# Performance work log

Hardware: AMD Instinct MI355X
Metric: run time of the kernel (lower is better)

## Reference

```python
import jax, jax.numpy as jnp
import numpy as np

DIM = 1024
NUM_HEADS = 16
HEAD_DIM = DIM // NUM_HEADS

def setup_inputs() -> dict:
    key = jax.random.key(0)
    ks = jax.random.split(key, 5)
    s = 1.0 / np.sqrt(DIM)
    x = jax.random.normal(ks[0], (2, 2048, DIM), dtype=jnp.float32)
    W_qkv = jax.random.uniform(ks[1], (DIM, 3 * DIM), dtype=jnp.float32, minval=-s, maxval=s)
    b_qkv = jax.random.uniform(ks[2], (3 * DIM,), dtype=jnp.float32, minval=-s, maxval=s)
    W_out = jax.random.uniform(ks[3], (DIM, DIM), dtype=jnp.float32, minval=-s, maxval=s)
    b_out = jax.random.uniform(ks[4], (DIM,), dtype=jnp.float32, minval=-s, maxval=s)
    return {"x": x, "W_qkv": W_qkv, "b_qkv": b_qkv, "W_out": W_out, "b_out": b_out}

def reference(x, W_qkv, b_qkv, W_out, b_out):
    B, S, _ = x.shape
    qkv = x @ W_qkv + b_qkv                       # [B,S,3*dim]
    q, k, v = jnp.split(qkv, 3, axis=-1)
    # [B,S,dim] -> [B,H,S,hd]
    def to_heads(t):
        return t.reshape(B, S, NUM_HEADS, HEAD_DIM).transpose(0, 2, 1, 3)
    q, k, v = to_heads(q), to_heads(k), to_heads(v)
    scale = HEAD_DIM ** -0.5
    scores = jnp.einsum('bhqd,bhkd->bhqk', q, k) * scale
    attn = jax.nn.softmax(scores, axis=-1)
    out = jnp.einsum('bhqk,bhkd->bhqd', attn, v)  # [B,H,S,hd]
    out = out.transpose(0, 2, 1, 3).reshape(B, S, DIM)
    return out @ W_out + b_out
```

## Files before the change

### kernel.cpp

```cpp
#include <hip/hip_runtime.h>
#include <math.h>

#define DIMM    1024
#define NHEADS  16
#define HDIM    64
#define BATCH   2
#define SEQ     2048
#define ROWS    (BATCH*SEQ)

typedef _Float16 f16x8 __attribute__((ext_vector_type(8)));
typedef _Float16 f16x4 __attribute__((ext_vector_type(4)));
typedef float    f32x4 __attribute__((ext_vector_type(4)));
typedef float    f32x16 __attribute__((ext_vector_type(16)));

__device__ inline void gl_lds16(const void* g, void* l) {
    __builtin_amdgcn_global_load_lds(
        (const __attribute__((address_space(1))) void*)g,
        (__attribute__((address_space(3))) void*)l, 16, 0, 0);
}

static __device__ inline f16x8 mkfrag(unsigned a, unsigned b, unsigned c, unsigned d) {
    union { unsigned u[4]; f16x8 v; } x;
    x.u[0] = a; x.u[1] = b; x.u[2] = c; x.u[3] = d;
    return x.v;
}

__device__ void tcvt64(const float* __restrict__ in, _Float16* __restrict__ out,
                       int K, int N, int k0, int n0, float (*tile)[65], int t)
{
    {
        const int c4 = (t & 15) * 4;
        const int r  = t >> 4;
        #pragma unroll
        for (int i = 0; i < 4; i++) {
            const int rr = r + 16 * i;
            float4 v = *(const float4*)(in + (size_t)(k0 + rr) * N + n0 + c4);
            tile[rr][c4] = v.x; tile[rr][c4 + 1] = v.y;
            tile[rr][c4 + 2] = v.z; tile[rr][c4 + 3] = v.w;
        }
    }
    __syncthreads();
    #pragma unroll
    for (int i = 0; i < 2; i++) {
        const int seg = t + 256 * i;
        const int n   = seg >> 3;
        const int kc  = (seg & 7) * 8;
        f16x8 o;
        #pragma unroll
        for (int j = 0; j < 8; j++) o[j] = (_Float16)tile[kc + j][n];
        *(f16x8*)(out + (size_t)(n0 + n) * K + k0 + kc) = o;
    }
}

__global__ __launch_bounds__(256)
void prep_kernel(const float* __restrict__ x, const float* __restrict__ Wqkv,
                 const float* __restrict__ Wout, _Float16* __restrict__ xh,
                 _Float16* __restrict__ wqkvt, _Float16* __restrict__ woutt)
{
    __shared__ float tile[64][65];
    const int bx = blockIdx.x;
    const int t  = threadIdx.x;
    if (bx < 2048) {
        const int i = bx * 256 + t;
        const float4 a = *(const float4*)(x + (size_t)i * 8);
        const float4 b = *(const float4*)(x + (size_t)i * 8 + 4);
        f16x8 o;
        o[0] = (_Float16)a.x; o[1] = (_Float16)a.y; o[2] = (_Float16)a.z; o[3] = (_Float16)a.w;
        o[4] = (_Float16)b.x; o[5] = (_Float16)b.y; o[6] = (_Float16)b.z; o[7] = (_Float16)b.w;
        *(f16x8*)(xh + (size_t)i * 8) = o;
    } else if (bx < 2816) {
        const int id = bx - 2048;
        const int gx = id % 48, gy = id / 48;
        tcvt64(Wqkv, wqkvt, DIMM, 3 * DIMM, gy * 64, gx * 64, tile, t);
    } else {
        const int id = bx - 2816;
        const int gx = id & 15, gy = id >> 4;
        tcvt64(Wout, woutt, DIMM, DIMM, gy * 64, gx * 64, tile, t);
    }
}

__global__ __launch_bounds__(512)
void hgemm256_kernel(const _Float16* __restrict__ A, const _Float16* __restrict__ Bt,
                     const float* __restrict__ bias, _Float16* __restrict__ C,
                     _Float16* __restrict__ vtg, int N, int K)
{
    __shared__ __align__(16) _Float16 lds[65536];

    const int t    = threadIdx.x;
    const int w    = t >> 6, lane = t & 63;
    const int l31  = lane & 31;
    const int hf   = lane >> 5;
    const int l7   = lane & 7;
    const int wm   = w >> 2;
    const int wn   = w & 3;
    const int row0 = blockIdx.y * 256, col0 = blockIdx.x * 256;

    f32x16 acc[4][2];
    #pragma unroll
    for (int mi = 0; mi < 4; mi++)
        #pragma unroll
        for (int ni = 0; ni < 2; ni++)
            #pragma unroll
            for (int r = 0; r < 16; r++) acc[mi][ni][r] = 0.f;

    const _Float16* gA[4];
    const _Float16* gB[4];
    int sofs[4];
    #pragma unroll
    for (int j = 0; j < 4; j++) {
        const int s   = t + 512 * j;
        const int row = s >> 3;
        const int kb  = (s & 7) ^ (row & 7);
        gA[j] = A  + (size_t)(row0 + row) * K + kb * 8;
        gB[j] = Bt + (size_t)(col0 + row) * K + kb * 8;
        sofs[j] = s * 8;
    }

    #pragma unroll
    for (int j = 0; j < 4; j++) gl_lds16(gA[j], lds + sofs[j]);
    #pragma unroll
    for (int j = 0; j < 4; j++) gl_lds16(gB[j], lds + 32768 + sofs[j]);
    #pragma unroll
    for (int j = 0; j < 4; j++) { gA[j] += 64; gB[j] += 64; }

    const int niter = K >> 6;
    #pragma unroll 1
    for (int it = 0; it < niter; it++) {
        const int cur = it & 1;
        __syncthreads();

        if (it + 1 < niter) {
            const int nxt = cur ^ 1;
            #pragma unroll
            for (int j = 0; j < 4; j++) gl_lds16(gA[j], lds + nxt * 16384 + sofs[j]);
            #pragma unroll
            for (int j = 0; j < 4; j++) gl_lds16(gB[j], lds + 32768 + nxt * 16384 + sofs[j]);
            #pragma unroll
            for (int j = 0; j < 4; j++) { gA[j] += 64; gB[j] += 64; }
        }

        const _Float16* AsC = lds + cur * 16384;
        const _Float16* BsC = lds + 32768 + cur * 16384;
        #pragma unroll
        for (int ks = 0; ks < 4; ks++) {
            const int pseg = ((ks * 2 + hf) ^ l7) * 8;
            f16x8 bf0 = *(const f16x8*)(BsC + (wn * 64 +      l31) * 64 + pseg);
            f16x8 bf1 = *(const f16x8*)(BsC + (wn * 64 + 32 + l31) * 64 + pseg);
            #pragma unroll
            for (int mi = 0; mi < 4; mi++) {
                f16x8 af = *(const f16x8*)(AsC + (wm * 128 + mi * 32 + l31) * 64 + pseg);
                acc[mi][0] = __builtin_amdgcn_mfma_f32_32x32x16_f16(af, bf0, acc[mi][0], 0, 0, 0);
                acc[mi][1] = __builtin_amdgcn_mfma_f32_32x32x16_f16(af, bf1, acc[mi][1], 0, 0, 0);
            }
        }
    }

    float bv[2];
    #pragma unroll
    for (int ni = 0; ni < 2; ni++) bv[ni] = bias[col0 + wn * 64 + ni * 32 + l31];

    if (blockIdx.x < 8) {
        #pragma unroll
        for (int mi = 0; mi < 4; mi++)
            #pragma unroll
            for (int ni = 0; ni < 2; ni++) {
                const int col = col0 + wn * 64 + ni * 32 + l31;
                #pragma unroll
                for (int r = 0; r < 16; r++) {
                    const int row = row0 + wm * 128 + mi * 32 + (r & 3) + 8 * (r >> 2) + 4 * hf;
                    C[(size_t)row * N + col] = (_Float16)(acc[mi][ni][r] + bv[ni]);
                }
            }
        return;
    }

    __syncthreads();
    #pragma unroll
    for (int mi = 0; mi < 4; mi++)
        #pragma unroll
        for (int ni = 0; ni < 2; ni++) {
            const int coll = wn * 64 + ni * 32 + l31;
            #pragma unroll
            for (int rq = 0; rq < 4; rq++) {
                f16x4 o;
                #pragma unroll
                for (int ri = 0; ri < 4; ri++) o[ri] = (_Float16)(acc[mi][ni][rq * 4 + ri] + bv[ni]);
                const int sidx = rq + 4 * mi + 16 * wm;
                *(f16x4*)(lds + coll * 256 + ((sidx ^ (coll & 31)) << 3) + 4 * hf) = o;
            }
        }
    __syncthreads();
    {
        const int cl   = t >> 1;
        const int half = t & 1;
        const int head = ((blockIdx.x - 8) << 2) + (cl >> 6);
        const int dv   = cl & 63;
        const int bb   = blockIdx.y >> 3;
        const int key0 = (blockIdx.y & 7) * 256 + half * 128;
        _Float16* dst = vtg + ((size_t)(bb * 16 + head) * 64 + dv) * SEQ + key0;
        #pragma unroll
        for (int c = 0; c < 16; c++) {
            const int cs = half * 16 + c;
            *(f16x8*)(dst + c * 8) = *(const f16x8*)(lds + cl * 256 + ((cs ^ (cl & 31)) << 3));
        }
    }
}

__global__ __launch_bounds__(256)
void hgemm_out_kernel(const _Float16* __restrict__ A, const _Float16* __restrict__ Bt,
                      const float* __restrict__ bias, float* __restrict__ Cout,
                      int N, int K)
{
    constexpr int BM = 64, MI = 2;
    __shared__ _Float16 As[2][BM * 64];
    __shared__ _Float16 Bs[2][128 * 64];

    const int t    = threadIdx.x;
    const int w    = t >> 6, lane = t & 63;
    const int quad = lane >> 4, l16 = lane & 15;
    const int wr   = w >> 1, wc = w & 1;
    const int row0 = blockIdx.y * BM, col0 = blockIdx.x * 128;
    const int sw   = l16 & 7;

    f32x4 acc[MI][4];
    #pragma unroll
    for (int i = 0; i < MI; i++)
        #pragma unroll
        for (int j = 0; j < 4; j++)
            #pragma unroll
            for (int r = 0; r < 4; r++) acc[i][j][r] = 0.f;

    const _Float16* gA[MI];
    int aofs[MI];
    #pragma unroll
    for (int j = 0; j < MI; j++) {
        const int s   = t + 256 * j;
        const int row = s >> 3;
        const int kb  = (s & 7) ^ (row & 7);
        gA[j] = A + (size_t)(row0 + row) * K + kb * 8;
        aofs[j] = s * 8;
    }
    const _Float16* gB[4];
    int bofs[4];
    #pragma unroll
    for (int j = 0; j < 4; j++) {
        const int s   = t + 256 * j;
        const int row = s >> 3;
        const int kb  = (s & 7) ^ (row & 7);
        gB[j] = Bt + (size_t)(col0 + row) * K + kb * 8;
        bofs[j] = s * 8;
    }

    #pragma unroll
    for (int j = 0; j < MI; j++) gl_lds16(gA[j], &As[0][aofs[j]]);
    #pragma unroll
    for (int j = 0; j < 4; j++)  gl_lds16(gB[j], &Bs[0][bofs[j]]);
    #pragma unroll
    for (int j = 0; j < MI; j++) gA[j] += 64;
    #pragma unroll
    for (int j = 0; j < 4; j++)  gB[j] += 64;

    const int niter = K >> 6;
    #pragma unroll 1
    for (int it = 0; it < niter; it++) {
        const int cur = it & 1;
        __syncthreads();

        if (it + 1 < niter) {
            const int nxt = cur ^ 1;
            #pragma unroll
            for (int j = 0; j < MI; j++) gl_lds16(gA[j], &As[nxt][aofs[j]]);
            #pragma unroll
            for (int j = 0; j < 4; j++)  gl_lds16(gB[j], &Bs[nxt][bofs[j]]);
            #pragma unroll
            for (int j = 0; j < MI; j++) gA[j] += 64;
            #pragma unroll
            for (int j = 0; j < 4; j++)  gB[j] += 64;
        }

        const _Float16* AsC = &As[cur][0];
        const _Float16* BsC = &Bs[cur][0];
        f16x8 af[MI][2], bf[4][2];
        #pragma unroll
        for (int i = 0; i < MI; i++) {
            const int arow = wr * (BM / 2) + i * 16 + l16;
            #pragma unroll
            for (int hh = 0; hh < 2; hh++)
                af[i][hh] = *(const f16x8*)(AsC + (arow * 8 + ((hh * 4 + quad) ^ sw)) * 8);
        }
        #pragma unroll
        for (int j = 0; j < 4; j++) {
            const int brow = wc * 64 + j * 16 + l16;
            #pragma unroll
            for (int hh = 0; hh < 2; hh++)
                bf[j][hh] = *(const f16x8*)(BsC + (brow * 8 + ((hh * 4 + quad) ^ sw)) * 8);
        }
        #pragma unroll
        for (int i = 0; i < MI; i++)
            #pragma unroll
            for (int j = 0; j < 4; j++) {
                acc[i][j] = __builtin_amdgcn_mfma_f32_16x16x32_f16(af[i][0], bf[j][0], acc[i][j], 0, 0, 0);
                acc[i][j] = __builtin_amdgcn_mfma_f32_16x16x32_f16(af[i][1], bf[j][1], acc[i][j], 0, 0, 0);
            }
    }

    #pragma unroll
    for (int j = 0; j < 4; j++) {
        const int col = col0 + wc * 64 + j * 16 + l16;
        const float bv = bias[col];
        #pragma unroll
        for (int i = 0; i < MI; i++) {
            const int row = row0 + wr * (BM / 2) + i * 16 + quad * 4;
            #pragma unroll
            for (int r = 0; r < 4; r++)
                Cout[(size_t)(row + r) * N + col] = acc[i][j][r] + bv;
        }
    }
}

__global__ __launch_bounds__(256, 4)
void flash_attn_kernel(const _Float16* __restrict__ qkv,
                       const _Float16* __restrict__ vtg,
                       _Float16* __restrict__ out)
{
    const int lin = blockIdx.y * 32 + blockIdx.x;
    const int bh  = (lin & 7) * 4 + (lin >> 8);
    const int qt  = (lin >> 3) & 31;
    const int b  = bh >> 4, hd = bh & 15;
    const int t    = threadIdx.x;
    const int w    = t >> 6;
    const int lane = t & 63;
    const int qg   = w >> 1;
    const int kh   = w & 1;
    const int l31  = lane & 31;
    const int hf   = lane >> 5;
    const int l7   = lane & 7;

    __shared__ __align__(16) _Float16 Ks [2][64 * 64];
    __shared__ __align__(16) _Float16 Vts[2][64 * 64];

    const int q0 = qt * 64;
    const size_t rstr = 3 * DIMM;
    const _Float16* qbase = qkv + (size_t)b * SEQ * rstr;

    f16x8 qf[4];
    {
        const _Float16* qrow = qbase + (size_t)(q0 + qg * 32 + l31) * rstr + hd * HDIM;
        #pragma unroll
        for (int dd = 0; dd < 4; dd++)
            qf[dd] = *(const f16x8*)(qrow + dd * 16 + hf * 8);
    }

    f32x16 Oacc[2];
    #pragma unroll
    for (int dh = 0; dh < 2; dh++)
        #pragma unroll
        for (int r = 0; r < 16; r++) Oacc[dh][r] = 0.f;
    float lrow = 0.f;

    const int seg0 = t, seg1 = t + 256;
    const int r0 = seg0 >> 3, lb0 = (seg0 & 7) ^ (r0 & 7);
    const int r1 = seg1 >> 3, lb1 = (seg1 & 7) ^ (r1 & 7);
    const _Float16* gK0 = qbase + (size_t)r0 * rstr + DIMM + hd * HDIM + lb0 * 8;
    const _Float16* gK1 = qbase + (size_t)r1 * rstr + DIMM + hd * HDIM + lb1 * 8;
    const _Float16* gV0 = vtg + ((size_t)bh * 64 + r0) * SEQ + lb0 * 8;
    const _Float16* gV1 = vtg + ((size_t)bh * 64 + r1) * SEQ + lb1 * 8;

    gl_lds16(gK0, &Ks [0][seg0 * 8]);
    gl_lds16(gK1, &Ks [0][seg1 * 8]);
    gl_lds16(gV0, &Vts[0][seg0 * 8]);
    gl_lds16(gV1, &Vts[0][seg1 * 8]);

    #pragma unroll 2
    for (int k0 = 0; k0 < SEQ; k0 += 64) {
        const int cur = (k0 >> 6) & 1;
        const _Float16* KsC  = &Ks [cur][0];
        const _Float16* VtsC = &Vts[cur][0];

        __syncthreads();

        f32x16 sacc;
        #pragma unroll
        for (int r = 0; r < 16; r++) sacc[r] = 0.f;
        __builtin_amdgcn_s_setprio(1);
        #pragma unroll
        for (int dd = 0; dd < 4; dd++) {
            f16x8 kf = *(const f16x8*)(KsC + (kh * 32 + l31) * 64 + (((dd * 2 + hf) ^ l7) * 8));
            sacc = __builtin_amdgcn_mfma_f32_32x32x16_f16(kf, qf[dd], sacc, 0, 0, 0);
        }
        __builtin_amdgcn_s_setprio(0);

        if (k0 + 64 < SEQ) {
            const int nxt = cur ^ 1;
            gl_lds16(gK0 + (size_t)(k0 + 64) * rstr, &Ks [nxt][seg0 * 8]);
            gl_lds16(gK1 + (size_t)(k0 + 64) * rstr, &Ks [nxt][seg1 * 8]);
            gl_lds16(gV0 + (k0 + 64),                &Vts[nxt][seg0 * 8]);
            gl_lds16(gV1 + (k0 + 64),                &Vts[nxt][seg1 * 8]);
        }

        float e[16];
        #pragma unroll
        for (int r = 0; r < 16; r++) {
            const float xx = sacc[r] * 0.18033688011112042f;
            float ee;
            asm("v_exp_f32 %0, %1" : "=v"(ee) : "v"(xx));
            e[r] = ee;
            lrow += ee;
        }

        unsigned w01 = __builtin_bit_cast(unsigned, __builtin_amdgcn_cvt_pkrtz(e[0],  e[1]));
        unsigned w23 = __builtin_bit_cast(unsigned, __builtin_amdgcn_cvt_pkrtz(e[2],  e[3]));
        unsigned w45 = __builtin_bit_cast(unsigned, __builtin_amdgcn_cvt_pkrtz(e[4],  e[5]));
        unsigned w67 = __builtin_bit_cast(unsigned, __builtin_amdgcn_cvt_pkrtz(e[6],  e[7]));
        unsigned w89 = __builtin_bit_cast(unsigned, __builtin_amdgcn_cvt_pkrtz(e[8],  e[9]));
        unsigned wab = __builtin_bit_cast(unsigned, __builtin_amdgcn_cvt_pkrtz(e[10], e[11]));
        unsigned wcd = __builtin_bit_cast(unsigned, __builtin_amdgcn_cvt_pkrtz(e[12], e[13]));
        unsigned wef = __builtin_bit_cast(unsigned, __builtin_amdgcn_cvt_pkrtz(e[14], e[15]));
        unsigned p00 = w01, p02 = w45;
        asm("v_permlane32_swap_b32 %0, %1" : "+v"(p00), "+v"(p02));
        unsigned p01 = w23, p03 = w67;
        asm("v_permlane32_swap_b32 %0, %1" : "+v"(p01), "+v"(p03));
        unsigned p10 = w89, p12 = wcd;
        asm("v_permlane32_swap_b32 %0, %1" : "+v"(p10), "+v"(p12));
        unsigned p11 = wab, p13 = wef;
        asm("v_permlane32_swap_b32 %0, %1" : "+v"(p11), "+v"(p13));
        f16x8 pa0 = mkfrag(p00, p01, p02, p03);
        f16x8 pa1 = mkfrag(p10, p11, p12, p13);

        __builtin_amdgcn_s_setprio(1);
        #pragma unroll
        for (int dh = 0; dh < 2; dh++) {
            const _Float16* vrow = VtsC + (dh * 32 + l31) * 64;
            f16x8 vf0 = *(const f16x8*)(vrow + (((kh * 4 + 0 + hf) ^ l7) * 8));
            f16x8 vf1 = *(const f16x8*)(vrow + (((kh * 4 + 2 + hf) ^ l7) * 8));
            Oacc[dh] = __builtin_amdgcn_mfma_f32_32x32x16_f16(pa0, vf0, Oacc[dh], 0, 0, 0);
            Oacc[dh] = __builtin_amdgcn_mfma_f32_32x32x16_f16(pa1, vf1, Oacc[dh], 0, 0, 0);
        }
        __builtin_amdgcn_s_setprio(0);
    }

    float lsum = lrow + __shfl_xor(lrow, 32);
    __syncthreads();
    float* Obuf = (float*)&Ks[0][0];
    float* lbuf = (float*)&Vts[0][0];
    if (kh) {
        #pragma unroll
        for (int dh = 0; dh < 2; dh++)
            #pragma unroll
            for (int r = 0; r < 16; r++) {
                const int q = (r & 3) + 8 * (r >> 2) + 4 * hf;
                Obuf[(qg * 32 + q) * 64 + dh * 32 + l31] = Oacc[dh][r];
            }
        if (lane < 32) lbuf[qg * 32 + lane] = lsum;
    }
    __syncthreads();
    if (!kh) {
        const float dnrec = 1.f / (lsum + lbuf[qg * 32 + l31]);
        float dq[16];
        #pragma unroll
        for (int r = 0; r < 16; r++)
            dq[r] = __shfl(dnrec, (r & 3) + 8 * (r >> 2) + 4 * hf);
        #pragma unroll
        for (int dh = 0; dh < 2; dh++)
            #pragma unroll
            for (int r = 0; r < 16; r++) {
                const int q = (r & 3) + 8 * (r >> 2) + 4 * hf;
                const float v = (Oacc[dh][r] + Obuf[(qg * 32 + q) * 64 + dh * 32 + l31])
                                * dq[r];
                out[(size_t)(b * SEQ + q0 + qg * 32 + q) * DIMM + hd * HDIM + dh * 32 + l31] =
                    (_Float16)v;
            }
    }
}

extern "C" void kernel_launch(void* const* d_in, const int* in_sizes, int n_in,
                              void* d_out, int out_size, void* d_ws, size_t ws_size,
                              hipStream_t stream)
{
    const float* x    = (const float*)d_in[0];
    const float* Wqkv = (const float*)d_in[1];
    const float* bqkv = (const float*)d_in[2];
    const float* Wout = (const float*)d_in[3];
    const float* bout = (const float*)d_in[4];
    float* out = (float*)d_out;

    _Float16* qkvh  = (_Float16*)d_ws;
    _Float16* attnh = qkvh  + (size_t)ROWS * 3 * DIMM;
    _Float16* xh    = attnh + (size_t)ROWS * DIMM;
    _Float16* wqkvt = xh    + (size_t)ROWS * DIMM;
    _Float16* woutt = wqkvt + (size_t)3 * DIMM * DIMM;
    _Float16* vtg   = woutt + (size_t)DIMM * DIMM;

    prep_kernel<<<3072, 256, 0, stream>>>(x, Wqkv, Wout, xh, wqkvt, woutt);
    {
        dim3 grid(3 * DIMM / 256, ROWS / 256);
        hgemm256_kernel<<<grid, 512, 0, stream>>>(xh, wqkvt, bqkv, qkvh, vtg, 3 * DIMM, DIMM);
    }
    {
        dim3 grid(SEQ / 64, BATCH * NHEADS);
        flash_attn_kernel<<<grid, 256, 0, stream>>>(qkvh, vtg, attnh);
    }
    {
        dim3 grid(DIMM / 128, ROWS / 64);
        hgemm_out_kernel<<<grid, 256, 0, stream>>>(attnh, woutt, bout, out, DIMM, DIMM);
    }
}
```

Baseline: 188.3 us.

## Fuse fp32-to-fp16 activation conversion into QKV GEMM and use fdot2 row sums

The separate x-to-fp16 conversion pass is removed from the prep kernel. The QKV GEMM now loads fp32 activations straight into registers, converts them, and writes them to LDS after the MFMA loop, replacing the direct global-to-LDS load for the A operand. This saves a full write and re-read of the fp16 activation buffer, at the cost of more register pressure and VALU/LDS-store work inside the GEMM loop. Separately, the attention softmax row sum is now accumulated with packed fp16 fdot2 on the already converted values instead of 16 scalar fp32 adds.

```diff
diff --git a/kernel.cpp b/kernel.cpp
--- a/kernel.cpp
+++ b/kernel.cpp
@@ -10,6 +10,7 @@
 
 typedef _Float16 f16x8 __attribute__((ext_vector_type(8)));
 typedef _Float16 f16x4 __attribute__((ext_vector_type(4)));
+typedef _Float16 h2    __attribute__((ext_vector_type(2)));
 typedef float    f32x4 __attribute__((ext_vector_type(4)));
 typedef float    f32x16 __attribute__((ext_vector_type(16)));
 
@@ -23,6 +24,13 @@
     union { unsigned u[4]; f16x8 v; } x;
     x.u[0] = a; x.u[1] = b; x.u[2] = c; x.u[3] = d;
     return x.v;
+}
+static __device__ inline f16x8 cvt8(const float4& a, const float4& b) {
+    unsigned u0 = __builtin_bit_cast(unsigned, __builtin_amdgcn_cvt_pkrtz(a.x, a.y));
+    unsigned u1 = __builtin_bit_cast(unsigned, __builtin_amdgcn_cvt_pkrtz(a.z, a.w));
+    unsigned u2 = __builtin_bit_cast(unsigned, __builtin_amdgcn_cvt_pkrtz(b.x, b.y));
+    unsigned u3 = __builtin_bit_cast(unsigned, __builtin_amdgcn_cvt_pkrtz(b.z, b.w));
+    return mkfrag(u0, u1, u2, u3);
 }
 
 __device__ void tcvt64(const float* __restrict__ in, _Float16* __restrict__ out,
@@ -53,34 +61,24 @@
 }
 
 __global__ __launch_bounds__(256)
-void prep_kernel(const float* __restrict__ x, const float* __restrict__ Wqkv,
-                 const float* __restrict__ Wout, _Float16* __restrict__ xh,
+void prep_kernel(const float* __restrict__ Wqkv, const float* __restrict__ Wout,
                  _Float16* __restrict__ wqkvt, _Float16* __restrict__ woutt)
 {
     __shared__ float tile[64][65];
     const int bx = blockIdx.x;
     const int t  = threadIdx.x;
-    if (bx < 2048) {
-        const int i = bx * 256 + t;
-        const float4 a = *(const float4*)(x + (size_t)i * 8);
-        const float4 b = *(const float4*)(x + (size_t)i * 8 + 4);
-        f16x8 o;
-        o[0] = (_Float16)a.x; o[1] = (_Float16)a.y; o[2] = (_Float16)a.z; o[3] = (_Float16)a.w;
-        o[4] = (_Float16)b.x; o[5] = (_Float16)b.y; o[6] = (_Float16)b.z; o[7] = (_Float16)b.w;
-        *(f16x8*)(xh + (size_t)i * 8) = o;
-    } else if (bx < 2816) {
-        const int id = bx - 2048;
-        const int gx = id % 48, gy = id / 48;
+    if (bx < 768) {
+        const int gx = bx % 48, gy = bx / 48;
         tcvt64(Wqkv, wqkvt, DIMM, 3 * DIMM, gy * 64, gx * 64, tile, t);
     } else {
-        const int id = bx - 2816;
+        const int id = bx - 768;
         const int gx = id & 15, gy = id >> 4;
         tcvt64(Wout, woutt, DIMM, DIMM, gy * 64, gx * 64, tile, t);
     }
 }
 
 __global__ __launch_bounds__(512)
-void hgemm256_kernel(const _Float16* __restrict__ A, const _Float16* __restrict__ Bt,
+void hgemm256_kernel(const float* __restrict__ X, const _Float16* __restrict__ Bt,
                      const float* __restrict__ bias, _Float16* __restrict__ C,
                      _Float16* __restrict__ vtg, int N, int K)
 {
@@ -103,7 +101,7 @@
             #pragma unroll
             for (int r = 0; r < 16; r++) acc[mi][ni][r] = 0.f;
 
-    const _Float16* gA[4];
+    const float*    gAf[4];
     const _Float16* gB[4];
     int sofs[4];
     #pragma unroll
@@ -111,17 +109,25 @@
         const int s   = t + 512 * j;
         const int row = s >> 3;
         const int kb  = (s & 7) ^ (row & 7);
-        gA[j] = A  + (size_t)(row0 + row) * K + kb * 8;
-        gB[j] = Bt + (size_t)(col0 + row) * K + kb * 8;
+        gAf[j] = X  + (size_t)(row0 + row) * K + kb * 8;
+        gB[j]  = Bt + (size_t)(col0 + row) * K + kb * 8;
         sofs[j] = s * 8;
     }
 
-    #pragma unroll
-    for (int j = 0; j < 4; j++) gl_lds16(gA[j], lds + sofs[j]);
-    #pragma unroll
-    for (int j = 0; j < 4; j++) gl_lds16(gB[j], lds + 32768 + sofs[j]);
-    #pragma unroll
-    for (int j = 0; j < 4; j++) { gA[j] += 64; gB[j] += 64; }
+    {
+        float4 pa[4], pb[4];
+        #pragma unroll
+        for (int j = 0; j < 4; j++) {
+            pa[j] = *(const float4*)(gAf[j]);
+            pb[j] = *(const float4*)(gAf[j] + 4);
+        }
+        #pragma unroll
+        for (int j = 0; j < 4; j++) *(f16x8*)(lds + sofs[j]) = cvt8(pa[j], pb[j]);
+        #pragma unroll
+        for (int j = 0; j < 4; j++) gl_lds16(gB[j], lds + 32768 + sofs[j]);
+        #pragma unroll
+        for (int j = 0; j < 4; j++) { gAf[j] += 64; gB[j] += 64; }
+    }
 
     const int niter = K >> 6;
     #pragma unroll 1
@@ -129,14 +135,19 @@
         const int cur = it & 1;
         __syncthreads();
 
+        float4 pa[4], pb[4];
+        const int nxt = cur ^ 1;
         if (it + 1 < niter) {
-            const int nxt = cur ^ 1;
-            #pragma unroll
-            for (int j = 0; j < 4; j++) gl_lds16(gA[j], lds + nxt * 16384 + sofs[j]);
-            #pragma unroll
-            for (int j = 0; j < 4; j++) gl_lds16(gB[j], lds + 32768 + nxt * 16384 + sofs[j]);
-            #pragma unroll
-            for (int j = 0; j < 4; j++) { gA[j] += 64; gB[j] += 64; }
+            #pragma unroll
+            for (int j = 0; j < 4; j++) {
+                pa[j] = *(const float4*)(gAf[j]);
+                pb[j] = *(const float4*)(gAf[j] + 4);
+            }
+            #pragma unroll
+            for (int j = 0; j < 4; j++)
+                gl_lds16(gB[j], lds + 32768 + nxt * 16384 + sofs[j]);
+            #pragma unroll
+            for (int j = 0; j < 4; j++) { gAf[j] += 64; gB[j] += 64; }
         }
 
         const _Float16* AsC = lds + cur * 16384;
@@ -152,6 +163,12 @@
                 acc[mi][0] = __builtin_amdgcn_mfma_f32_32x32x16_f16(af, bf0, acc[mi][0], 0, 0, 0);
                 acc[mi][1] = __builtin_amdgcn_mfma_f32_32x32x16_f16(af, bf1, acc[mi][1], 0, 0, 0);
             }
+        }
+
+        if (it + 1 < niter) {
+            #pragma unroll
+            for (int j = 0; j < 4; j++)
+                *(f16x8*)(lds + nxt * 16384 + sofs[j]) = cvt8(pa[j], pb[j]);
         }
     }
 
@@ -357,6 +374,7 @@
         #pragma unroll
         for (int r = 0; r < 16; r++) Oacc[dh][r] = 0.f;
     float lrow = 0.f;
+    const h2 k1 = {(_Float16)1.f, (_Float16)1.f};
 
     const int seg0 = t, seg1 = t + 256;
     const int r0 = seg0 >> 3, lb0 = (seg0 & 7) ^ (r0 & 7);
@@ -405,7 +423,6 @@
             float ee;
             asm("v_exp_f32 %0, %1" : "=v"(ee) : "v"(xx));
             e[r] = ee;
-            lrow += ee;
         }
 
         unsigned w01 = __builtin_bit_cast(unsigned, __builtin_amdgcn_cvt_pkrtz(e[0],  e[1]));
@@ -416,6 +433,16 @@
         unsigned wab = __builtin_bit_cast(unsigned, __builtin_amdgcn_cvt_pkrtz(e[10], e[11]));
         unsigned wcd = __builtin_bit_cast(unsigned, __builtin_amdgcn_cvt_pkrtz(e[12], e[13]));
         unsigned wef = __builtin_bit_cast(unsigned, __builtin_amdgcn_cvt_pkrtz(e[14], e[15]));
+
+        lrow = __builtin_amdgcn_fdot2(__builtin_bit_cast(h2, w01), k1, lrow, false);
+        lrow = __builtin_amdgcn_fdot2(__builtin_bit_cast(h2, w23), k1, lrow, false);
+        lrow = __builtin_amdgcn_fdot2(__builtin_bit_cast(h2, w45), k1, lrow, false);
+        lrow = __builtin_amdgcn_fdot2(__builtin_bit_cast(h2, w67), k1, lrow, false);
+        lrow = __builtin_amdgcn_fdot2(__builtin_bit_cast(h2, w89), k1, lrow, false);
+        lrow = __builtin_amdgcn_fdot2(__builtin_bit_cast(h2, wab), k1, lrow, false);
+        lrow = __builtin_amdgcn_fdot2(__builtin_bit_cast(h2, wcd), k1, lrow, false);
+        lrow = __builtin_amdgcn_fdot2(__builtin_bit_cast(h2, wef), k1, lrow, false);
+
         unsigned p00 = w01, p02 = w45;
         asm("v_permlane32_swap_b32 %0, %1" : "+v"(p00), "+v"(p02));
         unsigned p01 = w23, p03 = w67;
@@ -491,10 +518,10 @@
     _Float16* woutt = wqkvt + (size_t)3 * DIMM * DIMM;
     _Float16* vtg   = woutt + (size_t)DIMM * DIMM;
 
-    prep_kernel<<<3072, 256, 0, stream>>>(x, Wqkv, Wout, xh, wqkvt, woutt);
+    prep_kernel<<<1024, 256, 0, stream>>>(Wqkv, Wout, wqkvt, woutt);
     {
         dim3 grid(3 * DIMM / 256, ROWS / 256);
-        hgemm256_kernel<<<grid, 512, 0, stream>>>(xh, wqkvt, bqkv, qkvh, vtg, 3 * DIMM, DIMM);
+        hgemm256_kernel<<<grid, 512, 0, stream>>>(x, wqkvt, bqkv, qkvh, vtg, 3 * DIMM, DIMM);
     }
     {
         dim3 grid(SEQ / 64, BATCH * NHEADS);
```

New measurement: 187.2 us. No clear change (-0.6%).
